# Kernel tuning notes

Measured on AMD Instinct MI355X. Metric: run time of the kernel, lower is better.

The kernel has to match this reference:

```python
import jax, jax.numpy as jnp
import numpy as np

N_NODES = 16384
N_EDGES = 524288
N_GRAPHS = 256
IN_CH = 128
H_CH = 128   # per-head channels
HEADS = 2
LAYER_DIM = HEADS * H_CH  # 256, concat=True
POOL_DIM = 3 * LAYER_DIM  # 768
OUT_CH = 1
NEG_SLOPE = 0.2


def setup_inputs() -> dict:
    key = jax.random.key(0)
    ks = jax.random.split(key, 20)
    s = lambda k, shape, fan: jax.random.normal(k, shape, jnp.float32) * (1.0 / np.sqrt(fan))
    inp = {
        "x": jax.random.normal(ks[0], (N_NODES, IN_CH), jnp.float32),
        "edge_index": jax.random.randint(ks[1], (2, N_EDGES), 0, N_NODES, jnp.int64),
        "batch": jnp.sort(jax.random.randint(ks[2], (N_NODES,), 0, N_GRAPHS, jnp.int64)),
        # GATv2 layer 1 (in=128)
        "Wl1": s(ks[3], (IN_CH, LAYER_DIM), IN_CH), "Wr1": s(ks[4], (IN_CH, LAYER_DIM), IN_CH),
        "att1": s(ks[5], (HEADS, H_CH), H_CH), "b1": jnp.zeros((LAYER_DIM,), jnp.float32),
        # GATv2 layer 2 (in=256)
        "Wl2": s(ks[6], (LAYER_DIM, LAYER_DIM), LAYER_DIM), "Wr2": s(ks[7], (LAYER_DIM, LAYER_DIM), LAYER_DIM),
        "att2": s(ks[8], (HEADS, H_CH), H_CH), "b2": jnp.zeros((LAYER_DIM,), jnp.float32),
        # GATv2 layer 3 (in=256)
        "Wl3": s(ks[9], (LAYER_DIM, LAYER_DIM), LAYER_DIM), "Wr3": s(ks[10], (LAYER_DIM, LAYER_DIM), LAYER_DIM),
        "att3": s(ks[11], (HEADS, H_CH), H_CH), "b3": jnp.zeros((LAYER_DIM,), jnp.float32),
        # FFN (dropout inactive at eval)
        "fW1": s(ks[12], (POOL_DIM, POOL_DIM), POOL_DIM), "fb1": jnp.zeros((POOL_DIM,), jnp.float32),
        "fW2": s(ks[13], (POOL_DIM, OUT_CH), POOL_DIM), "fb2": jnp.zeros((OUT_CH,), jnp.float32),
    }
    return inp


def _gatv2(x, src, dst, Wl, Wr, att, b):
    """PyG GATv2Conv: per-edge score a . LeakyReLU(Wl x_src + Wr x_dst),
    softmax over incoming edges per destination, weighted scatter-add of Wl x_src."""
    n = x.shape[0]
    xl = (x @ Wl).reshape(n, HEADS, H_CH)  # source messages
    xr = (x @ Wr).reshape(n, HEADS, H_CH)  # target query
    e = jax.nn.leaky_relu(xl[src] + xr[dst], NEG_SLOPE)          # [E,H,C]
    logits = jnp.einsum('ehc,hc->eh', e, att)                    # [E,H]
    m = jax.ops.segment_max(logits, dst, num_segments=n)         # per-dst max (self-loops guarantee nonempty)
    ev = jnp.exp(logits - m[dst])
    denom = jax.ops.segment_sum(ev, dst, num_segments=n)
    alpha = ev / denom[dst]                                       # [E,H]
    out = jax.ops.segment_sum(alpha[..., None] * xl[src], dst, num_segments=n)  # [N,H,C]
    return out.reshape(n, LAYER_DIM) + b


def reference(x, edge_index, batch, Wl1, Wr1, att1, b1, Wl2, Wr2, att2, b2,
              Wl3, Wr3, att3, b3, fW1, fb1, fW2, fb2):
    n = x.shape[0]
    loops = jnp.arange(n, dtype=edge_index.dtype)
    src = jnp.concatenate([edge_index[0], loops])  # add_self_loops=True default
    dst = jnp.concatenate([edge_index[1], loops])
    h1 = _gatv2(x, src, dst, Wl1, Wr1, att1, b1)
    h2 = _gatv2(h1, src, dst, Wl2, Wr2, att2, b2)
    h3 = _gatv2(h2, src, dst, Wl3, Wr3, att3, b3)
    pool = lambda h: jax.ops.segment_sum(h, batch, num_segments=N_GRAPHS)
    h = jnp.concatenate([pool(h1), pool(h2), pool(h3)], axis=1)   # [G,768]
    h = jax.nn.relu(h @ fW1 + fb1)
    return h @ fW2 + fb2                                           # [G,1]
```

## Files before the change

### kernel.cpp

```cpp
#include <hip/hip_runtime.h>

#define NNODES 16384
#define NEDGES 524288
#define NETOT  (NEDGES + NNODES)
#define NGRAPH 256

typedef __attribute__((ext_vector_type(8))) short short8;
typedef __attribute__((ext_vector_type(4))) float f32x4;

__device__ __forceinline__ float b2f(unsigned short u){
  union { unsigned int i; float f; } v; v.i = ((unsigned int)u) << 16; return v.f;
}
__device__ __forceinline__ unsigned short f2b(float f){
  union { float f; unsigned int i; } v; v.f = f;
  unsigned int r = v.i + 0x7FFFu + ((v.i >> 16) & 1u);
  return (unsigned short)(r >> 16);
}

__global__ void __launch_bounds__(256) zero_deg(int* __restrict__ deg){
  deg[blockIdx.x * 256 + threadIdx.x] = 0;
}

__global__ void __launch_bounds__(256) count_deg(const int* __restrict__ ei, int* __restrict__ deg){
  int i = blockIdx.x * 256 + threadIdx.x;
  int d = (i < NEDGES) ? ei[NEDGES + i] : (i - NEDGES);
  atomicAdd(&deg[d], 1);
}

__global__ void __launch_bounds__(1024) scan_deg(const int* __restrict__ deg,
                                                 int* __restrict__ row_off,
                                                 int* __restrict__ cursor){
  __shared__ int wsum[16];
  __shared__ int woff[16];
  __shared__ int carry_s;
  const int tid = threadIdx.x, lane = tid & 63, w = tid >> 6;
  if(tid == 0){ carry_s = 0; row_off[0] = 0; }
  __syncthreads();
  for(int base = 0; base < NNODES; base += 1024){
    int v = deg[base + tid];
    int x = v;
    #pragma unroll
    for(int o = 1; o < 64; o <<= 1){ int u = __shfl_up(x, o, 64); if(lane >= o) x += u; }
    if(lane == 63) wsum[w] = x;
    __syncthreads();
    if(w == 0){
      int t0 = (lane < 16) ? wsum[lane] : 0;
      int y = t0;
      #pragma unroll
      for(int o = 1; o < 16; o <<= 1){ int u = __shfl_up(y, o, 64); if(lane >= o) y += u; }
      if(lane < 16) woff[lane] = y - t0;
    }
    __syncthreads();
    int carry = carry_s;
    int incl = carry + woff[w] + x;
    row_off[base + tid + 1] = incl;
    cursor[base + tid] = incl - v;
    __syncthreads();
    if(tid == 1023) carry_s = incl;
    __syncthreads();
  }
}

__global__ void __launch_bounds__(256) fill_csr(const int* __restrict__ ei, int* __restrict__ cursor,
                                                int* __restrict__ col_src){
  int i = blockIdx.x * 256 + threadIdx.x;
  int s, d;
  if(i < NEDGES){ s = ei[i]; d = ei[NEDGES + i]; }
  else          { s = i - NEDGES; d = s; }
  int p = atomicAdd(&cursor[d], 1);
  col_src[p] = s;
}

__global__ void __launch_bounds__(256) convX(const float* __restrict__ x, unsigned short* __restrict__ xb){
  int i = blockIdx.x * 256 + threadIdx.x;
  xb[i] = f2b(x[i]);
}

template<int K>
__global__ void __launch_bounds__(256) convW(const float* __restrict__ Wl, const float* __restrict__ Wr,
                                             unsigned short* __restrict__ Wt){
  int i = blockIdx.x * 256 + threadIdx.x;
  int k = i >> 9, c = i & 511;
  float val = (c < 256) ? Wl[(size_t)k * 256 + c] : Wr[(size_t)k * 256 + (c - 256)];
  unsigned short hi = f2b(val);
  unsigned short lo = f2b(val - b2f(hi));
  Wt[(size_t)c * (2 * K) + k]     = hi;
  Wt[(size_t)c * (2 * K) + K + k] = lo;
}

template<int K>
__global__ void __launch_bounds__(256) gemm_xw(const unsigned short* __restrict__ A,
                                               const unsigned short* __restrict__ Wt,
                                               unsigned short* __restrict__ Cout){
  __shared__ unsigned short As[128][40];
  __shared__ unsigned short Bs[128][40];
  const int t = threadIdx.x;
  const int rowbase = blockIdx.x * 128;
  const int colbase = blockIdx.y * 128;
  const int wave = t >> 6, lane = t & 63;
  const int lrow = lane & 15, kg = lane >> 4;

  f32x4 acc[2][8] = {};

  for(int kt = 0; kt < 2 * K; kt += 32){
    const int ka = kt & (K - 1);
    {
      int oct = t & 3, r = t >> 2;
      const unsigned short* ga = A + (size_t)(rowbase + r) * K + ka + oct * 8;
      short8 v0 = *(const short8*)ga;
      short8 v1 = *(const short8*)(ga + 64 * K);
      *(short8*)(&As[r][oct * 8])      = v0;
      *(short8*)(&As[r + 64][oct * 8]) = v1;
    }
    {
      int n = t & 127, kh = (t >> 7) * 16;
      const unsigned short* gw = Wt + (size_t)(colbase + n) * (2 * K) + kt + kh;
      short8 v0 = *(const short8*)gw;
      short8 v1 = *(const short8*)(gw + 8);
      *(short8*)(&Bs[n][kh])     = v0;
      *(short8*)(&Bs[n][kh + 8]) = v1;
    }
    __syncthreads();
    short8 afrag[2], bfrag[8];
    afrag[0] = *(const short8*)(&As[wave * 32 + lrow][kg * 8]);
    afrag[1] = *(const short8*)(&As[wave * 32 + 16 + lrow][kg * 8]);
    #pragma unroll
    for(int fc = 0; fc < 8; fc++) bfrag[fc] = *(const short8*)(&Bs[fc * 16 + lrow][kg * 8]);
    #pragma unroll
    for(int rf = 0; rf < 2; rf++)
      #pragma unroll
      for(int fc = 0; fc < 8; fc++)
        acc[rf][fc] = __builtin_amdgcn_mfma_f32_16x16x32_bf16(afrag[rf], bfrag[fc], acc[rf][fc], 0, 0, 0);
    __syncthreads();
  }
  #pragma unroll
  for(int rf = 0; rf < 2; rf++)
    #pragma unroll
    for(int fc = 0; fc < 8; fc++)
      #pragma unroll
      for(int r = 0; r < 4; r++){
        int row = rowbase + wave * 32 + rf * 16 + kg * 4 + r;
        int col = colbase + fc * 16 + lrow;
        Cout[(size_t)row * 512 + col] = f2b(acc[rf][fc][r]);
      }
}

__global__ void __launch_bounds__(256) edge_agg(const unsigned short* __restrict__ xlb,
                                                const int* __restrict__ row_off,
                                                const int* __restrict__ col_src,
                                                const float* __restrict__ att,
                                                const float* __restrict__ bias,
                                                unsigned short* __restrict__ hout){
  const int n = (blockIdx.x * 256 + threadIdx.x) >> 6;
  const int lane = threadIdx.x & 63;
  const int eg = lane >> 5;
  const int c0 = (lane & 31) * 8;
  float xr[8], at[8];
  {
    const unsigned short* xp = xlb + (size_t)n * 512 + 256 + c0;
    ushort4 v0 = *(const ushort4*)xp, v1 = *(const ushort4*)(xp + 4);
    xr[0] = b2f(v0.x); xr[1] = b2f(v0.y); xr[2] = b2f(v0.z); xr[3] = b2f(v0.w);
    xr[4] = b2f(v1.x); xr[5] = b2f(v1.y); xr[6] = b2f(v1.z); xr[7] = b2f(v1.w);
    #pragma unroll
    for(int i = 0; i < 8; i++) at[i] = att[c0 + i];
  }
  float s = 0.f;
  float ac[8] = {};
  const int beg = row_off[n], end = row_off[n + 1];
  for(int ch = beg; ch < end; ch += 64){
    int idx = ch + lane;
    int si = (idx < end) ? col_src[idx] : 0;
    int cnt = end - ch; if(cnt > 64) cnt = 64;
    for(int k = 0; k < cnt; k += 2){
      int kk = k + eg;
      bool valid = kk < cnt;
      int src = __shfl(si, kk & 63);
      const unsigned short* gp = xlb + (size_t)src * 512 + c0;
      ushort4 v0 = *(const ushort4*)gp, v1 = *(const ushort4*)(gp + 4);
      float x0 = b2f(v0.x), x1 = b2f(v0.y), x2 = b2f(v0.z), x3 = b2f(v0.w);
      float x4 = b2f(v1.x), x5 = b2f(v1.y), x6 = b2f(v1.z), x7 = b2f(v1.w);
      float e, p;
      e = x0 + xr[0]; e = fmaxf(e, 0.2f * e); p = at[0] * e;
      e = x1 + xr[1]; e = fmaxf(e, 0.2f * e); p = fmaf(at[1], e, p);
      e = x2 + xr[2]; e = fmaxf(e, 0.2f * e); p = fmaf(at[2], e, p);
      e = x3 + xr[3]; e = fmaxf(e, 0.2f * e); p = fmaf(at[3], e, p);
      e = x4 + xr[4]; e = fmaxf(e, 0.2f * e); p = fmaf(at[4], e, p);
      e = x5 + xr[5]; e = fmaxf(e, 0.2f * e); p = fmaf(at[5], e, p);
      e = x6 + xr[6]; e = fmaxf(e, 0.2f * e); p = fmaf(at[6], e, p);
      e = x7 + xr[7]; e = fmaxf(e, 0.2f * e); p = fmaf(at[7], e, p);
      p += __shfl_xor(p, 1); p += __shfl_xor(p, 2);
      p += __shfl_xor(p, 4); p += __shfl_xor(p, 8);
      float pe = valid ? __expf(p) : 0.f;
      s += pe;
      ac[0] = fmaf(pe, x0, ac[0]); ac[1] = fmaf(pe, x1, ac[1]);
      ac[2] = fmaf(pe, x2, ac[2]); ac[3] = fmaf(pe, x3, ac[3]);
      ac[4] = fmaf(pe, x4, ac[4]); ac[5] = fmaf(pe, x5, ac[5]);
      ac[6] = fmaf(pe, x6, ac[6]); ac[7] = fmaf(pe, x7, ac[7]);
    }
  }
  s += __shfl_xor(s, 32);
  #pragma unroll
  for(int i = 0; i < 8; i++) ac[i] += __shfl_xor(ac[i], 32);
  if(eg == 0){
    float inv = 1.f / s;
    ushort4 o0, o1;
    o0.x = f2b(fmaf(ac[0], inv, bias[c0 + 0]));
    o0.y = f2b(fmaf(ac[1], inv, bias[c0 + 1]));
    o0.z = f2b(fmaf(ac[2], inv, bias[c0 + 2]));
    o0.w = f2b(fmaf(ac[3], inv, bias[c0 + 3]));
    o1.x = f2b(fmaf(ac[4], inv, bias[c0 + 4]));
    o1.y = f2b(fmaf(ac[5], inv, bias[c0 + 5]));
    o1.z = f2b(fmaf(ac[6], inv, bias[c0 + 6]));
    o1.w = f2b(fmaf(ac[7], inv, bias[c0 + 7]));
    *(ushort4*)(hout + (size_t)n * 256 + c0)     = o0;
    *(ushort4*)(hout + (size_t)n * 256 + c0 + 4) = o1;
  }
}

__device__ __forceinline__ int lbound(const int* __restrict__ a, int n, int v){
  int lo = 0, hi = n;
  while(lo < hi){ int mid = (lo + hi) >> 1; if(a[mid] < v) lo = mid + 1; else hi = mid; }
  return lo;
}

__global__ void __launch_bounds__(256) pool_accum(const unsigned short* __restrict__ h,
                                                  const int* __restrict__ batch,
                                                  float* __restrict__ pool, int slot){
  __shared__ float red[8][264];
  const int g = blockIdx.x, t = threadIdx.x;
  const int ng = t >> 5, c0 = (t & 31) * 8;
  const int lo = lbound(batch, NNODES, g);
  const int hi = lbound(batch, NNODES, g + 1);
  float a[8] = {};
  for(int node = lo + ng; node < hi; node += 8){
    const unsigned short* hp = h + (size_t)node * 256 + c0;
    ushort4 v0 = *(const ushort4*)hp, v1 = *(const ushort4*)(hp + 4);
    a[0] += b2f(v0.x); a[1] += b2f(v0.y); a[2] += b2f(v0.z); a[3] += b2f(v0.w);
    a[4] += b2f(v1.x); a[5] += b2f(v1.y); a[6] += b2f(v1.z); a[7] += b2f(v1.w);
  }
  #pragma unroll
  for(int i = 0; i < 8; i++) red[ng][c0 + i] = a[i];
  __syncthreads();
  float s = 0.f;
  #pragma unroll
  for(int i = 0; i < 8; i++) s += red[i][t];
  pool[(size_t)g * 768 + slot * 256 + t] = s;
}

__global__ void __launch_bounds__(256) ffn1(const float* __restrict__ pool,
                                            const float* __restrict__ fW1,
                                            const float* __restrict__ fb1,
                                            float* __restrict__ hidden){
  __shared__ float ap[32][65];
  __shared__ float ws[64][33];
  const int t = threadIdx.x;
  const int cb = blockIdx.x * 32;
  const int gb = blockIdx.y * 32;
  const int tc = t & 31, tg = t >> 5;
  float acc[4] = {};
  for(int kc = 0; kc < 768; kc += 64){
    {
      int g_l = t >> 3, j8 = (t & 7) * 8;
      const float* gp = pool + (size_t)(gb + g_l) * 768 + kc + j8;
      #pragma unroll
      for(int i = 0; i < 8; i++) ap[g_l][j8 + i] = gp[i];
    }
    {
      int c_l = t & 31, k0 = (t >> 5) * 8;
      #pragma unroll
      for(int i = 0; i < 8; i++) ws[k0 + i][c_l] = fW1[(size_t)(kc + k0 + i) * 768 + cb + c_l];
    }
    __syncthreads();
    #pragma unroll
    for(int k = 0; k < 64; k++){
      float w = ws[k][tc];
      #pragma unroll
      for(int i = 0; i < 4; i++) acc[i] = fmaf(ap[tg * 4 + i][k], w, acc[i]);
    }
    __syncthreads();
  }
  float b = fb1[cb + tc];
  #pragma unroll
  for(int i = 0; i < 4; i++)
    hidden[(size_t)(gb + tg * 4 + i) * 768 + cb + tc] = fmaxf(acc[i] + b, 0.f);
}

__global__ void __launch_bounds__(256) ffn2(const float* __restrict__ hidden,
                                            const float* __restrict__ fW2,
                                            const float* __restrict__ fb2,
                                            float* __restrict__ out){
  const int g = (blockIdx.x * 256 + threadIdx.x) >> 6;
  const int lane = threadIdx.x & 63;
  float p = 0.f;
  for(int i = lane; i < 768; i += 64) p += hidden[(size_t)g * 768 + i] * fW2[i];
  #pragma unroll
  for(int o = 32; o > 0; o >>= 1) p += __shfl_xor(p, o, 64);
  if(lane == 0) out[g] = p + fb2[0];
}

extern "C" void kernel_launch(void* const* d_in, const int* in_sizes, int n_in,
                              void* d_out, int out_size, void* d_ws, size_t ws_size,
                              hipStream_t stream){
  const float* x    = (const float*)d_in[0];
  const int* ei     = (const int*)d_in[1];
  const int* batch  = (const int*)d_in[2];
  const float* Wl[3]  = {(const float*)d_in[3],  (const float*)d_in[7],  (const float*)d_in[11]};
  const float* Wr[3]  = {(const float*)d_in[4],  (const float*)d_in[8],  (const float*)d_in[12]};
  const float* att[3] = {(const float*)d_in[5],  (const float*)d_in[9],  (const float*)d_in[13]};
  const float* bp[3]  = {(const float*)d_in[6],  (const float*)d_in[10], (const float*)d_in[14]};
  const float* fW1 = (const float*)d_in[15];
  const float* fb1 = (const float*)d_in[16];
  const float* fW2 = (const float*)d_in[17];
  const float* fb2 = (const float*)d_in[18];

  char* ws = (char*)d_ws;
  size_t off = 0;
  auto alloc = [&](size_t sz){ size_t p = off; off += (sz + 255) & ~(size_t)255; return p; };
  int* deg      = (int*)(ws + alloc((size_t)NNODES * 4));
  int* rowoff   = (int*)(ws + alloc((size_t)(NNODES + 1) * 4));
  int* cursor   = (int*)(ws + alloc((size_t)NNODES * 4));
  int* colsrc   = (int*)(ws + alloc((size_t)NETOT * 4));
  unsigned short* xb  = (unsigned short*)(ws + alloc((size_t)NNODES * 128 * 2));
  unsigned short* Wt  = (unsigned short*)(ws + alloc((size_t)512 * 512 * 2));
  unsigned short* xlb = (unsigned short*)(ws + alloc((size_t)NNODES * 512 * 2));
  unsigned short* hA  = (unsigned short*)(ws + alloc((size_t)NNODES * 256 * 2));
  unsigned short* hB  = (unsigned short*)(ws + alloc((size_t)NNODES * 256 * 2));
  float* pool   = (float*)(ws + alloc((size_t)NGRAPH * 768 * 4));
  float* hidden = (float*)(ws + alloc((size_t)NGRAPH * 768 * 4));

  zero_deg<<<NNODES / 256, 256, 0, stream>>>(deg);
  count_deg<<<NETOT / 256, 256, 0, stream>>>(ei, deg);
  scan_deg<<<1, 1024, 0, stream>>>(deg, rowoff, cursor);
  fill_csr<<<NETOT / 256, 256, 0, stream>>>(ei, cursor, colsrc);

  dim3 ggrid(NNODES / 128, 4);

  convX<<<NNODES * 128 / 256, 256, 0, stream>>>(x, xb);
  convW<128><<<128 * 512 / 256, 256, 0, stream>>>(Wl[0], Wr[0], Wt);
  gemm_xw<128><<<ggrid, 256, 0, stream>>>(xb, Wt, xlb);
  edge_agg<<<NNODES / 4, 256, 0, stream>>>(xlb, rowoff, colsrc, att[0], bp[0], hA);
  pool_accum<<<NGRAPH, 256, 0, stream>>>(hA, batch, pool, 0);

  convW<256><<<256 * 512 / 256, 256, 0, stream>>>(Wl[1], Wr[1], Wt);
  gemm_xw<256><<<ggrid, 256, 0, stream>>>(hA, Wt, xlb);
  edge_agg<<<NNODES / 4, 256, 0, stream>>>(xlb, rowoff, colsrc, att[1], bp[1], hB);
  pool_accum<<<NGRAPH, 256, 0, stream>>>(hB, batch, pool, 1);

  convW<256><<<256 * 512 / 256, 256, 0, stream>>>(Wl[2], Wr[2], Wt);
  gemm_xw<256><<<ggrid, 256, 0, stream>>>(hB, Wt, xlb);
  edge_agg<<<NNODES / 4, 256, 0, stream>>>(xlb, rowoff, colsrc, att[2], bp[2], hA);
  pool_accum<<<NGRAPH, 256, 0, stream>>>(hA, batch, pool, 2);

  ffn1<<<dim3(768 / 32, NGRAPH / 32), 256, 0, stream>>>(pool, fW1, fb1, hidden);
  ffn2<<<NGRAPH / 4, 256, 0, stream>>>(hidden, fW2, fb2, (float*)d_out);
}
```

Before: 318.3 us.

## Drop split-bf16 weights, parallelize degree scan, pack edge aggregation math

Weights are now converted to a single bf16 value instead of a hi/lo split pair, which halves the GEMM K loop and the weight buffer at the cost of weight precision. The single-block serial degree scan becomes a three-kernel multi-block scan. Edge aggregation and pooling now use 128-bit loads and two-wide float vectors so the compiler can emit packed FP32 math. This cuts GEMM and ALU work but lowers numeric accuracy and adds two kernel launches.

```diff
diff --git a/kernel.cpp b/kernel.cpp
--- a/kernel.cpp
+++ b/kernel.cpp
@@ -7,6 +7,7 @@
 
 typedef __attribute__((ext_vector_type(8))) short short8;
 typedef __attribute__((ext_vector_type(4))) float f32x4;
+typedef __attribute__((ext_vector_type(2))) float f32x2;
 
 __device__ __forceinline__ float b2f(unsigned short u){
   union { unsigned int i; float f; } v; v.i = ((unsigned int)u) << 16; return v.f;
@@ -16,6 +17,11 @@
   unsigned int r = v.i + 0x7FFFu + ((v.i >> 16) & 1u);
   return (unsigned short)(r >> 16);
 }
+__device__ __forceinline__ f32x2 unpack2(unsigned int u){
+  union { unsigned int i; float f; } lo, hi;
+  lo.i = u << 16; hi.i = u & 0xFFFF0000u;
+  f32x2 r; r[0] = lo.f; r[1] = hi.f; return r;
+}
 
 __global__ void __launch_bounds__(256) zero_deg(int* __restrict__ deg){
   deg[blockIdx.x * 256 + threadIdx.x] = 0;
@@ -27,38 +33,41 @@
   atomicAdd(&deg[d], 1);
 }
 
-__global__ void __launch_bounds__(1024) scan_deg(const int* __restrict__ deg,
-                                                 int* __restrict__ row_off,
-                                                 int* __restrict__ cursor){
-  __shared__ int wsum[16];
-  __shared__ int woff[16];
-  __shared__ int carry_s;
-  const int tid = threadIdx.x, lane = tid & 63, w = tid >> 6;
-  if(tid == 0){ carry_s = 0; row_off[0] = 0; }
+__global__ void __launch_bounds__(256) scan1(const int* __restrict__ deg,
+                                             int* __restrict__ incl, int* __restrict__ bsum){
+  __shared__ int ws[4];
+  const int b = blockIdx.x, t = threadIdx.x, lane = t & 63, w = t >> 6;
+  int v = deg[b * 256 + t];
+  int x = v;
+  #pragma unroll
+  for(int o = 1; o < 64; o <<= 1){ int u = __shfl_up(x, o, 64); if(lane >= o) x += u; }
+  if(lane == 63) ws[w] = x;
   __syncthreads();
-  for(int base = 0; base < NNODES; base += 1024){
-    int v = deg[base + tid];
-    int x = v;
-    #pragma unroll
-    for(int o = 1; o < 64; o <<= 1){ int u = __shfl_up(x, o, 64); if(lane >= o) x += u; }
-    if(lane == 63) wsum[w] = x;
-    __syncthreads();
-    if(w == 0){
-      int t0 = (lane < 16) ? wsum[lane] : 0;
-      int y = t0;
-      #pragma unroll
-      for(int o = 1; o < 16; o <<= 1){ int u = __shfl_up(y, o, 64); if(lane >= o) y += u; }
-      if(lane < 16) woff[lane] = y - t0;
-    }
-    __syncthreads();
-    int carry = carry_s;
-    int incl = carry + woff[w] + x;
-    row_off[base + tid + 1] = incl;
-    cursor[base + tid] = incl - v;
-    __syncthreads();
-    if(tid == 1023) carry_s = incl;
-    __syncthreads();
-  }
+  int add = 0;
+  #pragma unroll
+  for(int j = 0; j < 4; j++) if(j < w) add += ws[j];
+  incl[b * 256 + t] = x + add;
+  if(t == 255) bsum[b] = x + add;
+}
+
+__global__ void __launch_bounds__(64) scan2(const int* __restrict__ bsum, int* __restrict__ boff){
+  const int t = threadIdx.x;
+  int v = bsum[t];
+  int x = v;
+  #pragma unroll
+  for(int o = 1; o < 64; o <<= 1){ int u = __shfl_up(x, o, 64); if(t >= o) x += u; }
+  boff[t] = x - v;
+}
+
+__global__ void __launch_bounds__(256) scan3(const int* __restrict__ deg, const int* __restrict__ incl,
+                                             const int* __restrict__ boff,
+                                             int* __restrict__ row_off, int* __restrict__ cursor){
+  const int b = blockIdx.x, t = threadIdx.x;
+  const int i = b * 256 + t;
+  int inc = incl[i] + boff[b];
+  row_off[i + 1] = inc;
+  cursor[i] = inc - deg[i];
+  if(i == 0) row_off[0] = 0;
 }
 
 __global__ void __launch_bounds__(256) fill_csr(const int* __restrict__ ei, int* __restrict__ cursor,
@@ -82,10 +91,7 @@
   int i = blockIdx.x * 256 + threadIdx.x;
   int k = i >> 9, c = i & 511;
   float val = (c < 256) ? Wl[(size_t)k * 256 + c] : Wr[(size_t)k * 256 + (c - 256)];
-  unsigned short hi = f2b(val);
-  unsigned short lo = f2b(val - b2f(hi));
-  Wt[(size_t)c * (2 * K) + k]     = hi;
-  Wt[(size_t)c * (2 * K) + K + k] = lo;
+  Wt[(size_t)c * K + k] = f2b(val);
 }
 
 template<int K>
@@ -102,11 +108,10 @@
 
   f32x4 acc[2][8] = {};
 
-  for(int kt = 0; kt < 2 * K; kt += 32){
-    const int ka = kt & (K - 1);
+  for(int kt = 0; kt < K; kt += 32){
     {
       int oct = t & 3, r = t >> 2;
-      const unsigned short* ga = A + (size_t)(rowbase + r) * K + ka + oct * 8;
+      const unsigned short* ga = A + (size_t)(rowbase + r) * K + kt + oct * 8;
       short8 v0 = *(const short8*)ga;
       short8 v1 = *(const short8*)(ga + 64 * K);
       *(short8*)(&As[r][oct * 8])      = v0;
@@ -114,7 +119,7 @@
     }
     {
       int n = t & 127, kh = (t >> 7) * 16;
-      const unsigned short* gw = Wt + (size_t)(colbase + n) * (2 * K) + kt + kh;
+      const unsigned short* gw = Wt + (size_t)(colbase + n) * K + kt + kh;
       short8 v0 = *(const short8*)gw;
       short8 v1 = *(const short8*)(gw + 8);
       *(short8*)(&Bs[n][kh])     = v0;
@@ -155,17 +160,17 @@
   const int lane = threadIdx.x & 63;
   const int eg = lane >> 5;
   const int c0 = (lane & 31) * 8;
-  float xr[8], at[8];
+  f32x2 xr0, xr1, xr2, xr3, at0, at1, at2, at3;
   {
-    const unsigned short* xp = xlb + (size_t)n * 512 + 256 + c0;
-    ushort4 v0 = *(const ushort4*)xp, v1 = *(const ushort4*)(xp + 4);
-    xr[0] = b2f(v0.x); xr[1] = b2f(v0.y); xr[2] = b2f(v0.z); xr[3] = b2f(v0.w);
-    xr[4] = b2f(v1.x); xr[5] = b2f(v1.y); xr[6] = b2f(v1.z); xr[7] = b2f(v1.w);
-    #pragma unroll
-    for(int i = 0; i < 8; i++) at[i] = att[c0 + i];
+    uint4 v = *(const uint4*)(xlb + (size_t)n * 512 + 256 + c0);
+    xr0 = unpack2(v.x); xr1 = unpack2(v.y); xr2 = unpack2(v.z); xr3 = unpack2(v.w);
+    at0 = *(const f32x2*)(att + c0);
+    at1 = *(const f32x2*)(att + c0 + 2);
+    at2 = *(const f32x2*)(att + c0 + 4);
+    at3 = *(const f32x2*)(att + c0 + 6);
   }
   float s = 0.f;
-  float ac[8] = {};
+  f32x2 ac0 = {0.f, 0.f}, ac1 = {0.f, 0.f}, ac2 = {0.f, 0.f}, ac3 = {0.f, 0.f};
   const int beg = row_off[n], end = row_off[n + 1];
   for(int ch = beg; ch < end; ch += 64){
     int idx = ch + lane;
@@ -173,45 +178,44 @@
     int cnt = end - ch; if(cnt > 64) cnt = 64;
     for(int k = 0; k < cnt; k += 2){
       int kk = k + eg;
-      bool valid = kk < cnt;
-      int src = __shfl(si, kk & 63);
-      const unsigned short* gp = xlb + (size_t)src * 512 + c0;
-      ushort4 v0 = *(const ushort4*)gp, v1 = *(const ushort4*)(gp + 4);
-      float x0 = b2f(v0.x), x1 = b2f(v0.y), x2 = b2f(v0.z), x3 = b2f(v0.w);
-      float x4 = b2f(v1.x), x5 = b2f(v1.y), x6 = b2f(v1.z), x7 = b2f(v1.w);
-      float e, p;
-      e = x0 + xr[0]; e = fmaxf(e, 0.2f * e); p = at[0] * e;
-      e = x1 + xr[1]; e = fmaxf(e, 0.2f * e); p = fmaf(at[1], e, p);
-      e = x2 + xr[2]; e = fmaxf(e, 0.2f * e); p = fmaf(at[2], e, p);
-      e = x3 + xr[3]; e = fmaxf(e, 0.2f * e); p = fmaf(at[3], e, p);
-      e = x4 + xr[4]; e = fmaxf(e, 0.2f * e); p = fmaf(at[4], e, p);
-      e = x5 + xr[5]; e = fmaxf(e, 0.2f * e); p = fmaf(at[5], e, p);
-      e = x6 + xr[6]; e = fmaxf(e, 0.2f * e); p = fmaf(at[6], e, p);
-      e = x7 + xr[7]; e = fmaxf(e, 0.2f * e); p = fmaf(at[7], e, p);
+      int src = __shfl(si, kk);
+      uint4 v = *(const uint4*)(xlb + (size_t)src * 512 + c0);
+      f32x2 x0 = unpack2(v.x), x1 = unpack2(v.y), x2 = unpack2(v.z), x3 = unpack2(v.w);
+      f32x2 e0 = x0 + xr0, e1 = x1 + xr1, e2 = x2 + xr2, e3 = x3 + xr3;
+      e0 = __builtin_elementwise_max(e0, e0 * 0.2f);
+      e1 = __builtin_elementwise_max(e1, e1 * 0.2f);
+      e2 = __builtin_elementwise_max(e2, e2 * 0.2f);
+      e3 = __builtin_elementwise_max(e3, e3 * 0.2f);
+      f32x2 p2 = e0 * at0;
+      p2 += e1 * at1;
+      p2 += e2 * at2;
+      p2 += e3 * at3;
+      float p = p2[0] + p2[1];
       p += __shfl_xor(p, 1); p += __shfl_xor(p, 2);
       p += __shfl_xor(p, 4); p += __shfl_xor(p, 8);
-      float pe = valid ? __expf(p) : 0.f;
+      float pe = (kk < cnt) ? __expf(p) : 0.f;
       s += pe;
-      ac[0] = fmaf(pe, x0, ac[0]); ac[1] = fmaf(pe, x1, ac[1]);
-      ac[2] = fmaf(pe, x2, ac[2]); ac[3] = fmaf(pe, x3, ac[3]);
-      ac[4] = fmaf(pe, x4, ac[4]); ac[5] = fmaf(pe, x5, ac[5]);
-      ac[6] = fmaf(pe, x6, ac[6]); ac[7] = fmaf(pe, x7, ac[7]);
+      f32x2 pe2 = {pe, pe};
+      ac0 += pe2 * x0; ac1 += pe2 * x1; ac2 += pe2 * x2; ac3 += pe2 * x3;
     }
   }
   s += __shfl_xor(s, 32);
   #pragma unroll
-  for(int i = 0; i < 8; i++) ac[i] += __shfl_xor(ac[i], 32);
+  for(int i = 0; i < 2; i++){
+    ac0[i] += __shfl_xor(ac0[i], 32); ac1[i] += __shfl_xor(ac1[i], 32);
+    ac2[i] += __shfl_xor(ac2[i], 32); ac3[i] += __shfl_xor(ac3[i], 32);
+  }
   if(eg == 0){
     float inv = 1.f / s;
     ushort4 o0, o1;
-    o0.x = f2b(fmaf(ac[0], inv, bias[c0 + 0]));
-    o0.y = f2b(fmaf(ac[1], inv, bias[c0 + 1]));
-    o0.z = f2b(fmaf(ac[2], inv, bias[c0 + 2]));
-    o0.w = f2b(fmaf(ac[3], inv, bias[c0 + 3]));
-    o1.x = f2b(fmaf(ac[4], inv, bias[c0 + 4]));
-    o1.y = f2b(fmaf(ac[5], inv, bias[c0 + 5]));
-    o1.z = f2b(fmaf(ac[6], inv, bias[c0 + 6]));
-    o1.w = f2b(fmaf(ac[7], inv, bias[c0 + 7]));
+    o0.x = f2b(fmaf(ac0[0], inv, bias[c0 + 0]));
+    o0.y = f2b(fmaf(ac0[1], inv, bias[c0 + 1]));
+    o0.z = f2b(fmaf(ac1[0], inv, bias[c0 + 2]));
+    o0.w = f2b(fmaf(ac1[1], inv, bias[c0 + 3]));
+    o1.x = f2b(fmaf(ac2[0], inv, bias[c0 + 4]));
+    o1.y = f2b(fmaf(ac2[1], inv, bias[c0 + 5]));
+    o1.z = f2b(fmaf(ac3[0], inv, bias[c0 + 6]));
+    o1.w = f2b(fmaf(ac3[1], inv, bias[c0 + 7]));
     *(ushort4*)(hout + (size_t)n * 256 + c0)     = o0;
     *(ushort4*)(hout + (size_t)n * 256 + c0 + 4) = o1;
   }
@@ -231,15 +235,15 @@
   const int ng = t >> 5, c0 = (t & 31) * 8;
   const int lo = lbound(batch, NNODES, g);
   const int hi = lbound(batch, NNODES, g + 1);
-  float a[8] = {};
+  f32x2 a0 = {0.f,0.f}, a1 = {0.f,0.f}, a2 = {0.f,0.f}, a3 = {0.f,0.f};
   for(int node = lo + ng; node < hi; node += 8){
-    const unsigned short* hp = h + (size_t)node * 256 + c0;
-    ushort4 v0 = *(const ushort4*)hp, v1 = *(const ushort4*)(hp + 4);
-    a[0] += b2f(v0.x); a[1] += b2f(v0.y); a[2] += b2f(v0.z); a[3] += b2f(v0.w);
-    a[4] += b2f(v1.x); a[5] += b2f(v1.y); a[6] += b2f(v1.z); a[7] += b2f(v1.w);
-  }
-  #pragma unroll
-  for(int i = 0; i < 8; i++) red[ng][c0 + i] = a[i];
+    uint4 v = *(const uint4*)(h + (size_t)node * 256 + c0);
+    a0 += unpack2(v.x); a1 += unpack2(v.y); a2 += unpack2(v.z); a3 += unpack2(v.w);
+  }
+  red[ng][c0 + 0] = a0[0]; red[ng][c0 + 1] = a0[1];
+  red[ng][c0 + 2] = a1[0]; red[ng][c0 + 3] = a1[1];
+  red[ng][c0 + 4] = a2[0]; red[ng][c0 + 5] = a2[1];
+  red[ng][c0 + 6] = a3[0]; red[ng][c0 + 7] = a3[1];
   __syncthreads();
   float s = 0.f;
   #pragma unroll
@@ -320,8 +324,11 @@
   int* rowoff   = (int*)(ws + alloc((size_t)(NNODES + 1) * 4));
   int* cursor   = (int*)(ws + alloc((size_t)NNODES * 4));
   int* colsrc   = (int*)(ws + alloc((size_t)NETOT * 4));
+  int* incl     = (int*)(ws + alloc((size_t)NNODES * 4));
+  int* bsum     = (int*)(ws + alloc(64 * 4));
+  int* boff     = (int*)(ws + alloc(64 * 4));
   unsigned short* xb  = (unsigned short*)(ws + alloc((size_t)NNODES * 128 * 2));
-  unsigned short* Wt  = (unsigned short*)(ws + alloc((size_t)512 * 512 * 2));
+  unsigned short* Wt  = (unsigned short*)(ws + alloc((size_t)512 * 256 * 2));
   unsigned short* xlb = (unsigned short*)(ws + alloc((size_t)NNODES * 512 * 2));
   unsigned short* hA  = (unsigned short*)(ws + alloc((size_t)NNODES * 256 * 2));
   unsigned short* hB  = (unsigned short*)(ws + alloc((size_t)NNODES * 256 * 2));
@@ -330,7 +337,9 @@
 
   zero_deg<<<NNODES / 256, 256, 0, stream>>>(deg);
   count_deg<<<NETOT / 256, 256, 0, stream>>>(ei, deg);
-  scan_deg<<<1, 1024, 0, stream>>>(deg, rowoff, cursor);
+  scan1<<<NNODES / 256, 256, 0, stream>>>(deg, incl, bsum);
+  scan2<<<1, 64, 0, stream>>>(bsum, boff);
+  scan3<<<NNODES / 256, 256, 0, stream>>>(deg, incl, boff, rowoff, cursor);
   fill_csr<<<NETOT / 256, 256, 0, stream>>>(ei, cursor, colsrc);
 
   dim3 ggrid(NNODES / 128, 4);
```

Measured after the change: 290.1 us. 1.1x faster.
